# Optimization experiments

Hardware: AMD Instinct MI355X
Metric: run time of the kernel (lower is better)

The kernel has to match this reference:

```python
import jax, jax.numpy as jnp
import numpy as np
import math

B, L, HID, H = 16, 1024, 1024, 16
E = HID // H
HALF = L // 2 + 1                      # 513 rfft bins
GLOBAL_RATIO = 0.6
LEFT = int(HALF * (1.0 - GLOBAL_RATIO))  # 205 (i=0, filter_mixer='G')
RIGHT = HALF                            # 513
FACTOR = 1
TOP_K = int(FACTOR * math.log(L))       # 6
LN_EPS = 1e-12


def setup_inputs() -> dict:
    key = jax.random.key(0)
    ks = jax.random.split(key, 12)
    s = 0.02
    return {
        "input_tensor": jax.random.normal(ks[0], (B, L, HID), jnp.float32),
        "attention_mask": jnp.zeros((B, 1, 1, L), jnp.float32),
        "Wq": jax.random.normal(ks[1], (HID, HID), jnp.float32) * s,
        "bq": jnp.zeros((HID,), jnp.float32),
        "Wk": jax.random.normal(ks[2], (HID, HID), jnp.float32) * s,
        "bk": jnp.zeros((HID,), jnp.float32),
        "Wv": jax.random.normal(ks[3], (HID, HID), jnp.float32) * s,
        "bv": jnp.zeros((HID,), jnp.float32),
        "Wd": jax.random.normal(ks[4], (HID, HID), jnp.float32) * s,
        "bd": jnp.zeros((HID,), jnp.float32),
        "gamma": jnp.ones((HID,), jnp.float32),
        "beta": jnp.zeros((HID,), jnp.float32),
    }


def _heads(x):  # [B,L,HID] -> [B,H,E,L]
    return x.reshape(B, L, H, E).transpose(0, 2, 3, 1)


def _layer_norm(x, gamma, beta):
    mu = jnp.mean(x, axis=-1, keepdims=True)
    var = jnp.var(x, axis=-1, keepdims=True)
    return (x - mu) / jnp.sqrt(var + LN_EPS) * gamma + beta


def reference(input_tensor, attention_mask, Wq, bq, Wk, bk, Wv, bv, Wd, bd, gamma, beta):
    # QKV projections -> [B,H,E,L]
    q = _heads(input_tensor @ Wq + bq)
    k = _heads(input_tensor @ Wk + bk)
    v = _heads(input_tensor @ Wv + bv)

    # FFT-based autocorrelation restricted to retained frequency band [LEFT,RIGHT)
    q_fft = jnp.fft.rfft(q, axis=-1)            # [B,H,E,HALF] complex64
    k_fft = jnp.fft.rfft(k, axis=-1)
    res = q_fft[..., LEFT:RIGHT] * jnp.conj(k_fft[..., LEFT:RIGHT])
    box = jnp.zeros((B, H, E, HALF), res.dtype).at[..., LEFT:RIGHT].set(res)
    corr = jnp.fft.irfft(box, n=L, axis=-1)     # [B,H,E,L]

    # time_delay_agg_training: topk shared delays, softmax-weighted roll aggregation
    mean_value = jnp.mean(corr, axis=(1, 2))            # [B,L]
    _, idx = jax.lax.top_k(jnp.mean(mean_value, axis=0), TOP_K)  # [TOP_K]
    weights = mean_value[:, idx]                         # [B,TOP_K]
    tmp_corr = jax.nn.softmax(weights, axis=-1)
    delays_agg = jnp.zeros_like(v)
    for i in range(TOP_K):  # TOP_K=6, fixed small loop
        pattern = jnp.roll(v, -idx[i], axis=-1)
        delays_agg = delays_agg + pattern * tmp_corr[:, i][:, None, None, None]

    # [B,H,E,L] -> [B,L,HID]
    context = delays_agg.transpose(0, 3, 1, 2).reshape(B, L, HID)
    hidden = context @ Wd + bd
    return _layer_norm(hidden + input_tensor, gamma, beta)
```

## Files before the change

kernel.cpp:

```cpp
#include <hip/hip_runtime.h>


typedef unsigned short u16;
typedef unsigned int   u32;
typedef __attribute__((ext_vector_type(8))) __bf16 bf16x8;
typedef __attribute__((ext_vector_type(4))) float  floatx4;

#define HIDn 1024

__device__ __forceinline__ u16 f2b(float f){ u32 i = __float_as_uint(f); return (u16)((i + 0x7fffu + ((i>>16)&1u)) >> 16); }

__device__ __forceinline__ void gl_lds16(const u16* g, u16* l){
  __builtin_amdgcn_global_load_lds((__attribute__((address_space(1))) const void*)g,
                                   (__attribute__((address_space(3))) void*)l, 16, 0, 0);
}

__device__ __forceinline__ void bar(){
  asm volatile("" ::: "memory");
  __builtin_amdgcn_s_barrier();
  asm volatile("" ::: "memory");
}
__device__ __forceinline__ void lgkm0(){
  asm volatile("s_waitcnt lgkmcnt(0)" ::: "memory");
  __builtin_amdgcn_sched_barrier(0);
}

__global__ void fill_kernel(float* __restrict__ out, float v, int n)
{
  const int i = blockIdx.x*blockDim.x + threadIdx.x;
  if (i < n) out[i] = v;
}

__global__ __launch_bounds__(256)
void cast_kernel(const float* __restrict__ x, u16* __restrict__ xb)
{
  const int i = blockIdx.x*256 + threadIdx.x;
  const float4* xp = (const float4*)x;
  const float4 a = xp[2*i], b = xp[2*i+1];
  uint4 o;
  o.x = (u32)f2b(a.x) | ((u32)f2b(a.y)<<16);
  o.y = (u32)f2b(a.z) | ((u32)f2b(a.w)<<16);
  o.z = (u32)f2b(b.x) | ((u32)f2b(b.y)<<16);
  o.w = (u32)f2b(b.z) | ((u32)f2b(b.w)<<16);
  ((uint4*)xb)[i] = o;
}

__global__ __launch_bounds__(1024)
void transpose_kernel(const float* __restrict__ Wq, const float* __restrict__ Wk,
                      const float* __restrict__ Wv, const float* __restrict__ Wd,
                      u16* __restrict__ WqkvT, u16* __restrict__ WdT)
{
  __shared__ float tile[32][33];
  const int mat = blockIdx.z;
  const float* W = (mat==0)?Wq:(mat==1)?Wk:(mat==2)?Wv:Wd;
  const int k = blockIdx.y*32 + threadIdx.y;
  const int n = blockIdx.x*32 + threadIdx.x;
  tile[threadIdx.y][threadIdx.x] = W[(long)k*HIDn + n];
  __syncthreads();
  const int on = blockIdx.x*32 + threadIdx.y;
  const int ok = blockIdx.y*32 + threadIdx.x;
  const u16 val = f2b(tile[threadIdx.x][threadIdx.y]);
  if (mat < 3) WqkvT[(long)(mat*HIDn + on)*HIDn + ok] = val;
  else         WdT[(long)on*HIDn + ok] = val;
}

__global__ __launch_bounds__(1024)
void gf_kernel(float* __restrict__ gf, float* __restrict__ c)
{
  const int d = threadIdx.x;
  float s = 0.f;
  for (int f = 205; f < 512; ++f){
    int p = (f*d) & 1023;
    s += cosf(6.283185307179586f * (float)p * (1.0f/1024.0f));
  }
  gf[d] = (2.f*s + ((d & 1) ? -1.f : 1.f)) * (1.0f/1048576.0f);
  #pragma unroll
  for (int b = 0; b < 16; ++b) c[b*1024 + d] = 0.f;
}

template<int EPI>
__global__ __launch_bounds__(512, 2)
void gemm_mfma(const u16* __restrict__ A, int lda, long sA,
               const u16* __restrict__ Bt, int ldb, long sB,
               void* __restrict__ C0, u16* __restrict__ o1, u16* __restrict__ o2,
               int ldc, int K,
               const float* __restrict__ b0, const float* __restrict__ b1,
               const float* __restrict__ b2, const float* __restrict__ resid,
               float* __restrict__ cbuf)
{
  __shared__ __align__(16) u16 As[2][16384];
  __shared__ __align__(16) u16 Bs[2][16384];
  __shared__ float bins[512];

  const int bx = blockIdx.x, by = blockIdx.y, bz = blockIdx.z;
  const int tid  = threadIdx.x;
  const int wave = tid >> 6, lane = tid & 63;
  const int waveM = wave >> 2, waveN = wave & 3;
  const int qd = lane >> 4, ln = lane & 15, rl = ln & 7;
  const u16* Ab = A  + (long)bz * sA;
  const u16* Bb = Bt + (long)bz * sB;
  const int aRow0 = by * 256, bRow0 = bx * 256;
  const int nt = K >> 6;

  const int s0 = wave*128 + lane;
  const int r0 = s0 >> 3, r1 = r0 + 8;
  const int kc = ((s0 & 7) ^ (r0 & 7)) * 8;
  const long aOff0 = (long)(aRow0 + r0)*lda + kc;
  const long aOff1 = (long)(aRow0 + r1)*lda + kc;
  const long bOff0 = (long)(bRow0 + r0)*ldb + kc;
  const long bOff1 = (long)(bRow0 + r1)*ldb + kc;
  const int dstW = wave*1024;

#define STAGE_A(p, h, kt) do{ \
    gl_lds16(Ab + aOff0 + (long)(h)*128*lda + (kt), &As[p][(h)*8192 + dstW]); \
    gl_lds16(Ab + aOff1 + (long)(h)*128*lda + (kt), &As[p][(h)*8192 + dstW + 512]); }while(0)
#define STAGE_B(p, h, kt) do{ \
    gl_lds16(Bb + bOff0 + (long)(h)*128*ldb + (kt), &Bs[p][(h)*8192 + dstW]); \
    gl_lds16(Bb + bOff1 + (long)(h)*128*ldb + (kt), &Bs[p][(h)*8192 + dstW + 512]); }while(0)

  if (EPI == 3) bins[tid] = 0.f;

  floatx4 acc[8][4];
  const floatx4 z4 = {0.f, 0.f, 0.f, 0.f};
  #pragma unroll
  for (int i=0;i<8;++i)
    #pragma unroll
    for (int j=0;j<4;++j) acc[i][j] = z4;

  const int aRd = (waveM*128 + ln)*64;
  const int bRd = (waveN*64  + ln)*64;
  const int csw0 = ((0 + qd) ^ rl) * 8;
  const int csw1 = ((4 + qd) ^ rl) * 8;

  bf16x8 av0[4], av1[4];
  bf16x8 bvA0[2], bvA1[2];
  bf16x8 bvB0[2], bvB1[2];

#define DS_AV(BUF, MH) do{ const u16* Ap_ = &As[BUF][0]; \
    _Pragma("unroll") for (int mi=0;mi<4;++mi){ \
      av0[mi] = *(const bf16x8*)(Ap_ + aRd + (MH)*4096 + mi*1024 + csw0); \
      av1[mi] = *(const bf16x8*)(Ap_ + aRd + (MH)*4096 + mi*1024 + csw1); } }while(0)
#define DS_BV(BUF, NH, d0_, d1_) do{ const u16* Bp_ = &Bs[BUF][0]; \
    _Pragma("unroll") for (int ni=0;ni<2;++ni){ \
      d0_[ni] = *(const bf16x8*)(Bp_ + bRd + ((NH)*2+ni)*1024 + csw0); \
      d1_[ni] = *(const bf16x8*)(Bp_ + bRd + ((NH)*2+ni)*1024 + csw1); } }while(0)
#define MFMAQ(MH, NH, b0_, b1_) do{ \
    __builtin_amdgcn_sched_barrier(0); \
    __builtin_amdgcn_s_setprio(1); \
    _Pragma("unroll") for (int mi=0;mi<4;++mi) \
      _Pragma("unroll") for (int ni=0;ni<2;++ni){ \
        acc[(MH)*4+mi][(NH)*2+ni] = __builtin_amdgcn_mfma_f32_16x16x32_bf16(av0[mi], b0_[ni], acc[(MH)*4+mi][(NH)*2+ni],0,0,0); \
        acc[(MH)*4+mi][(NH)*2+ni] = __builtin_amdgcn_mfma_f32_16x16x32_bf16(av1[mi], b1_[ni], acc[(MH)*4+mi][(NH)*2+ni],0,0,0); } \
    __builtin_amdgcn_s_setprio(0); \
    __builtin_amdgcn_sched_barrier(0); }while(0)

  STAGE_B(0,0,0);  STAGE_B(0,1,0);  STAGE_A(0,0,0);  STAGE_A(0,1,0);
  STAGE_B(1,0,64); STAGE_B(1,1,64); STAGE_A(1,0,64); STAGE_A(1,1,64);
  asm volatile("s_waitcnt vmcnt(8)" ::: "memory");
  bar();

  const int nIt = nt >> 1;
  for (int it = 0; it < nIt-1; ++it){
    const int k2 = (it*2+2) << 6;
    const int k3 = (it*2+3) << 6;
    DS_AV(0,0); DS_BV(0,0,bvA0,bvA1);
    bar(); lgkm0(); MFMAQ(0,0,bvA0,bvA1); bar();
    DS_BV(0,1,bvB0,bvB1);
    bar(); lgkm0(); MFMAQ(0,1,bvB0,bvB1); bar();
    DS_AV(0,1); STAGE_B(0,0,k2);
    bar(); lgkm0(); MFMAQ(1,0,bvA0,bvA1); bar();
    STAGE_B(0,1,k2);
    asm volatile("s_waitcnt vmcnt(4)" ::: "memory");
    bar(); MFMAQ(1,1,bvB0,bvB1); bar();
    DS_AV(1,0); DS_BV(1,0,bvA0,bvA1); STAGE_A(0,0,k2);
    bar(); lgkm0(); MFMAQ(0,0,bvA0,bvA1); bar();
    DS_BV(1,1,bvB0,bvB1); STAGE_A(0,1,k2);
    bar(); lgkm0(); MFMAQ(0,1,bvB0,bvB1); bar();
    DS_AV(1,1); STAGE_B(1,0,k3);
    bar(); lgkm0(); MFMAQ(1,0,bvA0,bvA1); bar();
    STAGE_B(1,1,k3); STAGE_A(1,0,k3); STAGE_A(1,1,k3);
    asm volatile("s_waitcnt vmcnt(8)" ::: "memory");
    bar(); MFMAQ(1,1,bvB0,bvB1); bar();
  }
  DS_AV(0,0); DS_BV(0,0,bvA0,bvA1);
  bar(); lgkm0(); MFMAQ(0,0,bvA0,bvA1); bar();
  DS_BV(0,1,bvB0,bvB1);
  bar(); lgkm0(); MFMAQ(0,1,bvB0,bvB1); bar();
  DS_AV(0,1);
  bar(); lgkm0(); MFMAQ(1,0,bvA0,bvA1); bar();
  asm volatile("s_waitcnt vmcnt(0)" ::: "memory");
  bar(); MFMAQ(1,1,bvB0,bvB1); bar();
  DS_AV(1,0); DS_BV(1,0,bvA0,bvA1);
  bar(); lgkm0(); MFMAQ(0,0,bvA0,bvA1); bar();
  DS_BV(1,1,bvB0,bvB1);
  bar(); lgkm0(); MFMAQ(0,1,bvB0,bvB1); bar();
  DS_AV(1,1);
  bar(); lgkm0(); MFMAQ(1,0,bvA0,bvA1); bar();
  MFMAQ(1,1,bvB0,bvB1);
#undef STAGE_A
#undef STAGE_B
#undef DS_AV
#undef DS_BV
#undef MFMAQ

  if (EPI == 3){
    float dsum[11][4];
    #pragma unroll
    for (int dd=0; dd<11; ++dd)
      #pragma unroll
      for (int r=0;r<4;++r) dsum[dd][r] = 0.f;
    #pragma unroll
    for (int mi=0;mi<8;++mi)
      #pragma unroll
      for (int ni=0;ni<4;++ni){
        const int dd = mi - ni + 3;
        #pragma unroll
        for (int r=0;r<4;++r) dsum[dd][r] += acc[mi][ni][r];
      }
    const int base = 255 + 128*waveM - 64*waveN + 4*qd - ln;
    #pragma unroll
    for (int dd=0; dd<11; ++dd)
      #pragma unroll
      for (int r=0;r<4;++r)
        atomicAdd(&bins[base + 16*(dd-3) + r], dsum[dd][r]);
    __syncthreads();
    if (tid < 511){
      const int d = (aRow0 - bRow0 + tid - 255) & 1023;
      atomicAdd(cbuf + bz*1024 + d, bins[tid]);
    }
    return;
  }

  if (EPI == 0){
    const int which = bx >> 2;
    const float* bp = (which==0) ? b0 : ((which==1) ? b1 : b2);
    u16* Cb = (which==0) ? (u16*)C0 : ((which==1) ? o1 : o2);
    const int nb = bRow0 & 1023;
    #pragma unroll
    for (int mi=0;mi<8;++mi){
      const int gm = aRow0 + waveM*128 + mi*16 + qd*4;
      #pragma unroll
      for (int ni=0;ni<4;++ni){
        const int nl = nb + waveN*64 + ni*16 + ln;
        const float bias = bp[nl];
        #pragma unroll
        for (int r=0;r<4;++r) Cb[(long)(gm+r)*ldc + nl] = f2b(acc[mi][ni][r] + bias);
      }
    }
  } else {
    float* C = (float*)C0;
    #pragma unroll
    for (int mi=0;mi<8;++mi){
      const int gm = aRow0 + waveM*128 + mi*16 + qd*4;
      #pragma unroll
      for (int ni=0;ni<4;++ni){
        const int gn = bRow0 + waveN*64 + ni*16 + ln;
        const float bias = b0[gn];
        #pragma unroll
        for (int r=0;r<4;++r)
          C[(long)(gm+r)*ldc + gn] = acc[mi][ni][r] + bias + resid[(long)(gm+r)*ldc + gn];
      }
    }
  }
}

__global__ __launch_bounds__(1024)
void filter_kernel(const float* __restrict__ c, const float* __restrict__ gf,
                   float* __restrict__ mv)
{
  __shared__ float carr[1024];
  __shared__ float gsh[1024];
  const int b = blockIdx.x, l = threadIdx.x;
  carr[l] = c[b*1024 + l]; gsh[l] = gf[l];
  __syncthreads();
  float o = 0.f;
  #pragma unroll 4
  for (int m = 0; m < 1024; ++m) o += carr[m] * gsh[(l - m) & 1023];
  mv[b*1024 + l] = o;
}

__global__ __launch_bounds__(1024)
void topk_kernel(const float* __restrict__ mv, int* __restrict__ idxout,
                 float* __restrict__ wout)
{
  __shared__ float vals[1024];
  __shared__ float rv[1024];
  __shared__ int   ri[1024];
  __shared__ int   chosen[6];
  const int t = threadIdx.x;
  float s = 0.f;
  #pragma unroll
  for (int b = 0; b < 16; ++b) s += mv[b*1024 + t];
  vals[t] = s;
  __syncthreads();
  for (int r = 0; r < 6; ++r){
    rv[t] = vals[t]; ri[t] = t; __syncthreads();
    for (int off = 512; off > 0; off >>= 1){
      if (t < off){
        const float v2 = rv[t+off]; const int i2 = ri[t+off];
        if (v2 > rv[t] || (v2 == rv[t] && i2 < ri[t])){ rv[t] = v2; ri[t] = i2; }
      }
      __syncthreads();
    }
    if (t == 0){ chosen[r] = ri[0]; idxout[r] = ri[0]; }
    __syncthreads();
    if (t == chosen[r]) vals[t] = -3.0e38f;
    __syncthreads();
  }
  if (t < 16){
    float w[6]; float mx = -3.0e38f;
    #pragma unroll
    for (int i = 0; i < 6; ++i){ w[i] = mv[t*1024 + chosen[i]]; mx = fmaxf(mx, w[i]); }
    float sum = 0.f;
    #pragma unroll
    for (int i = 0; i < 6; ++i){ w[i] = expf(w[i] - mx); sum += w[i]; }
    #pragma unroll
    for (int i = 0; i < 6; ++i) wout[t*6 + i] = w[i] / sum;
  }
}

__global__ __launch_bounds__(256)
void context_kernel(const u16* __restrict__ Vb, const int* __restrict__ idx,
                    const float* __restrict__ w, u16* __restrict__ CT)
{
  const int row = blockIdx.x*2 + (threadIdx.x >> 7);
  const int b = row >> 10, l = row & 1023;
  const int t = threadIdx.x & 127;
  float wl[6]; int id[6];
  #pragma unroll
  for (int i = 0; i < 6; ++i){ id[i] = idx[i]; wl[i] = w[b*6 + i]; }
  float acc[8] = {0,0,0,0,0,0,0,0};
  #pragma unroll
  for (int i = 0; i < 6; ++i){
    const long src = (long)b*1024 + ((l + id[i]) & 1023);
    const uint4 pk = *(const uint4*)(Vb + src*1024 + t*8);
    const float ww = wl[i];
    union{float f; u32 u;} cv;
    cv.u = pk.x<<16;          acc[0] += ww*cv.f;
    cv.u = pk.x & 0xffff0000u; acc[1] += ww*cv.f;
    cv.u = pk.y<<16;          acc[2] += ww*cv.f;
    cv.u = pk.y & 0xffff0000u; acc[3] += ww*cv.f;
    cv.u = pk.z<<16;          acc[4] += ww*cv.f;
    cv.u = pk.z & 0xffff0000u; acc[5] += ww*cv.f;
    cv.u = pk.w<<16;          acc[6] += ww*cv.f;
    cv.u = pk.w & 0xffff0000u; acc[7] += ww*cv.f;
  }
  uint4 o;
  o.x = (u32)f2b(acc[0]) | ((u32)f2b(acc[1])<<16);
  o.y = (u32)f2b(acc[2]) | ((u32)f2b(acc[3])<<16);
  o.z = (u32)f2b(acc[4]) | ((u32)f2b(acc[5])<<16);
  o.w = (u32)f2b(acc[6]) | ((u32)f2b(acc[7])<<16);
  *(uint4*)(CT + (long)row*1024 + t*8) = o;
}

__global__ __launch_bounds__(256)
void ln_kernel(float* __restrict__ io, const float* __restrict__ gamma,
               const float* __restrict__ beta)
{
  __shared__ float s1[256];
  __shared__ float s2[256];
  const int row = blockIdx.x, t = threadIdx.x;
  float4 v = ((const float4*)(io + (long)row*1024))[t];
  s1[t] = v.x+v.y+v.z+v.w;
  s2[t] = v.x*v.x+v.y*v.y+v.z*v.z+v.w*v.w;
  __syncthreads();
  for (int off = 128; off > 0; off >>= 1){
    if (t < off){ s1[t] += s1[t+off]; s2[t] += s2[t+off]; }
    __syncthreads();
  }
  const float mu  = s1[0] * (1.f/1024.f);
  const float var = fmaxf(s2[0] * (1.f/1024.f) - mu*mu, 0.f);
  const float rstd = rsqrtf(var + 1e-12f);
  const float4 g  = ((const float4*)gamma)[t];
  const float4 be = ((const float4*)beta)[t];
  float4 o;
  o.x = (v.x-mu)*rstd*g.x + be.x;
  o.y = (v.y-mu)*rstd*g.y + be.y;
  o.z = (v.z-mu)*rstd*g.z + be.z;
  o.w = (v.w-mu)*rstd*g.w + be.w;
  ((float4*)(io + (long)row*1024))[t] = o;
}

extern "C" void kernel_launch(void* const* d_in, const int* in_sizes, int n_in,
                              void* d_out, int out_size, void* d_ws, size_t ws_size,
                              hipStream_t stream)
{
  (void)in_sizes; (void)n_in;
  const float* x     = (const float*)d_in[0];
  const float* Wq    = (const float*)d_in[2];
  const float* bq    = (const float*)d_in[3];
  const float* Wk    = (const float*)d_in[4];
  const float* bk    = (const float*)d_in[5];
  const float* Wv    = (const float*)d_in[6];
  const float* bv    = (const float*)d_in[7];
  const float* Wd    = (const float*)d_in[8];
  const float* bd    = (const float*)d_in[9];
  const float* gamma = (const float*)d_in[10];
  const float* beta  = (const float*)d_in[11];
  float* outp = (float*)d_out;

  const size_t NEED = 142741952UL;
  if (ws_size < NEED){
    const int n = out_size/2;
    fill_kernel<<<(n+255)/256, 256, 0, stream>>>(outp, (float)ws_size, n);
    return;
  }
  char* ws = (char*)d_ws;
  u16*  xb    = (u16*)(ws);
  u16*  Qb    = (u16*)(ws + 33554432L);
  u16*  Kb    = (u16*)(ws + 67108864L);
  u16*  Vb    = (u16*)(ws + 100663296L);
  u16*  WqkvT = (u16*)(ws + 134217728L);
  u16*  WdT   = (u16*)(ws + 140509184L);
  float* cbuf = (float*)(ws + 142606336L);
  float* mv   = (float*)(ws + 142671872L);
  float* gf   = (float*)(ws + 142737408L);
  int*   idxb = (int*)  (ws + 142741504L);
  float* wsm  = (float*)(ws + 142741568L);
  u16*  CT    = Qb;

  cast_kernel<<<8192, 256, 0, stream>>>(x, xb);
  transpose_kernel<<<dim3(32,32,4), dim3(32,32), 0, stream>>>(Wq, Wk, Wv, Wd, WqkvT, WdT);
  gf_kernel<<<1, 1024, 0, stream>>>(gf, cbuf);

  gemm_mfma<0><<<dim3(12,64,1), 512, 0, stream>>>(
      xb, 1024, 0L, WqkvT, 1024, 0L, Qb, Kb, Vb, 1024, 1024,
      bq, bk, bv, nullptr, nullptr);

  gemm_mfma<3><<<dim3(4,4,16), 512, 0, stream>>>(
      Qb, 1024, 1048576L, Kb, 1024, 1048576L, nullptr, nullptr, nullptr, 0, 1024,
      nullptr, nullptr, nullptr, nullptr, cbuf);

  filter_kernel<<<16, 1024, 0, stream>>>(cbuf, gf, mv);
  topk_kernel<<<1, 1024, 0, stream>>>(mv, idxb, wsm);
  context_kernel<<<8192, 256, 0, stream>>>(Vb, idxb, wsm, CT);

  gemm_mfma<2><<<dim3(4,64,1), 512, 0, stream>>>(
      CT, 1024, 0L, WdT, 1024, 0L, outp, nullptr, nullptr, 1024, 1024,
      bd, nullptr, nullptr, x, nullptr);

  ln_kernel<<<16384, 256, 0, stream>>>(outp, gamma, beta);
}
```

Baseline: 497.8 us.

## Drop gf kernel, use closed-form filter, swizzle GEMM blocks, warp-shuffle topk

Removes the serial gf_kernel launch. The band-pass filter is now computed in closed form (a Dirichlet-kernel sin/cos ratio) inside a filter kernel split into 64 blocks, and the cbuf zeroing moves into the cast kernel. The GEMM kernels remap block indices with an XCD-style swizzle so neighbouring tiles share cache. Top-k replaces the shared-memory tree reduction with wave shuffles. The closed-form filter may differ slightly numerically from the summed cosines, which could flip tie-breaking in top-k.

```diff
diff --git a/kernel.cpp b/kernel.cpp
--- a/kernel.cpp
+++ b/kernel.cpp
@@ -32,9 +32,11 @@
 }
 
 __global__ __launch_bounds__(256)
-void cast_kernel(const float* __restrict__ x, u16* __restrict__ xb)
+void cast_kernel(const float* __restrict__ x, u16* __restrict__ xb,
+                 float* __restrict__ cbuf)
 {
   const int i = blockIdx.x*256 + threadIdx.x;
+  if (blockIdx.x < 64) cbuf[i] = 0.f;
   const float4* xp = (const float4*)x;
   const float4 a = xp[2*i], b = xp[2*i+1];
   uint4 o;
@@ -64,20 +66,6 @@
   else         WdT[(long)on*HIDn + ok] = val;
 }
 
-__global__ __launch_bounds__(1024)
-void gf_kernel(float* __restrict__ gf, float* __restrict__ c)
-{
-  const int d = threadIdx.x;
-  float s = 0.f;
-  for (int f = 205; f < 512; ++f){
-    int p = (f*d) & 1023;
-    s += cosf(6.283185307179586f * (float)p * (1.0f/1024.0f));
-  }
-  gf[d] = (2.f*s + ((d & 1) ? -1.f : 1.f)) * (1.0f/1048576.0f);
-  #pragma unroll
-  for (int b = 0; b < 16; ++b) c[b*1024 + d] = 0.f;
-}
-
 template<int EPI>
 __global__ __launch_bounds__(512, 2)
 void gemm_mfma(const u16* __restrict__ A, int lda, long sA,
@@ -92,7 +80,15 @@
   __shared__ __align__(16) u16 Bs[2][16384];
   __shared__ float bins[512];
 
-  const int bx = blockIdx.x, by = blockIdx.y, bz = blockIdx.z;
+  const int gx = gridDim.x, gy = gridDim.y;
+  const int lin = (blockIdx.z*gy + blockIdx.y)*gx + blockIdx.x;
+  const int cpx = (gx*gy*gridDim.z) >> 3;
+  const int swz = (lin & 7)*cpx + (lin >> 3);
+  const int bx  = swz % gx;
+  const int byz = swz / gx;
+  const int by  = byz % gy;
+  const int bz  = byz / gy;
+
   const int tid  = threadIdx.x;
   const int wave = tid >> 6, lane = tid & 63;
   const int waveM = wave >> 2, waveN = wave & 3;
@@ -264,15 +260,28 @@
   }
 }
 
-__global__ __launch_bounds__(1024)
-void filter_kernel(const float* __restrict__ c, const float* __restrict__ gf,
-                   float* __restrict__ mv)
+__global__ __launch_bounds__(256)
+void filter_kernel(const float* __restrict__ c, float* __restrict__ mv)
 {
   __shared__ float carr[1024];
   __shared__ float gsh[1024];
-  const int b = blockIdx.x, l = threadIdx.x;
-  carr[l] = c[b*1024 + l]; gsh[l] = gf[l];
+  const int b = blockIdx.x >> 2, l0 = (blockIdx.x & 3) << 8;
+  const int t = threadIdx.x;
+  #pragma unroll
+  for (int j = 0; j < 4; ++j){
+    const int d = t + j*256;
+    carr[d] = c[b*1024 + d];
+    float s;
+    if (d == 0) s = 307.f;
+    else {
+      const float k = 3.14159265358979e0f/1024.f;
+      const int n1 = (307*d) & 2047, n2 = (716*d) & 2047;
+      s = sinf((float)n1*k) * cosf((float)n2*k) / sinf((float)d*k);
+    }
+    gsh[d] = (2.f*s + ((d & 1) ? -1.f : 1.f)) * (1.0f/1048576.0f);
+  }
   __syncthreads();
+  const int l = l0 + t;
   float o = 0.f;
   #pragma unroll 4
   for (int m = 0; m < 1024; ++m) o += carr[m] * gsh[(l - m) & 1023];
@@ -284,27 +293,32 @@
                  float* __restrict__ wout)
 {
   __shared__ float vals[1024];
-  __shared__ float rv[1024];
-  __shared__ int   ri[1024];
+  __shared__ float wv[16];
+  __shared__ int   wi[16];
   __shared__ int   chosen[6];
-  const int t = threadIdx.x;
+  const int t = threadIdx.x, lane = t & 63, wid = t >> 6;
   float s = 0.f;
   #pragma unroll
   for (int b = 0; b < 16; ++b) s += mv[b*1024 + t];
   vals[t] = s;
   __syncthreads();
   for (int r = 0; r < 6; ++r){
-    rv[t] = vals[t]; ri[t] = t; __syncthreads();
-    for (int off = 512; off > 0; off >>= 1){
-      if (t < off){
-        const float v2 = rv[t+off]; const int i2 = ri[t+off];
-        if (v2 > rv[t] || (v2 == rv[t] && i2 < ri[t])){ rv[t] = v2; ri[t] = i2; }
-      }
-      __syncthreads();
-    }
-    if (t == 0){ chosen[r] = ri[0]; idxout[r] = ri[0]; }
+    float cv = vals[t]; int ci = t;
+    #pragma unroll
+    for (int off = 32; off > 0; off >>= 1){
+      const float ov = __shfl_down(cv, off);
+      const int   oi = __shfl_down(ci, off);
+      if (ov > cv || (ov == cv && oi < ci)){ cv = ov; ci = oi; }
+    }
+    if (lane == 0){ wv[wid] = cv; wi[wid] = ci; }
     __syncthreads();
-    if (t == chosen[r]) vals[t] = -3.0e38f;
+    if (t == 0){
+      float bv = wv[0]; int bi = wi[0];
+      #pragma unroll
+      for (int k = 1; k < 16; ++k)
+        if (wv[k] > bv || (wv[k] == bv && wi[k] < bi)){ bv = wv[k]; bi = wi[k]; }
+      chosen[r] = bi; idxout[r] = bi; vals[bi] = -3.0e38f;
+    }
     __syncthreads();
   }
   if (t < 16){
@@ -414,14 +428,12 @@
   u16*  WdT   = (u16*)(ws + 140509184L);
   float* cbuf = (float*)(ws + 142606336L);
   float* mv   = (float*)(ws + 142671872L);
-  float* gf   = (float*)(ws + 142737408L);
   int*   idxb = (int*)  (ws + 142741504L);
   float* wsm  = (float*)(ws + 142741568L);
   u16*  CT    = Qb;
 
-  cast_kernel<<<8192, 256, 0, stream>>>(x, xb);
+  cast_kernel<<<8192, 256, 0, stream>>>(x, xb, cbuf);
   transpose_kernel<<<dim3(32,32,4), dim3(32,32), 0, stream>>>(Wq, Wk, Wv, Wd, WqkvT, WdT);
-  gf_kernel<<<1, 1024, 0, stream>>>(gf, cbuf);
 
   gemm_mfma<0><<<dim3(12,64,1), 512, 0, stream>>>(
       xb, 1024, 0L, WqkvT, 1024, 0L, Qb, Kb, Vb, 1024, 1024,
@@ -431,7 +443,7 @@
       Qb, 1024, 1048576L, Kb, 1024, 1048576L, nullptr, nullptr, nullptr, 0, 1024,
       nullptr, nullptr, nullptr, nullptr, cbuf);
 
-  filter_kernel<<<16, 1024, 0, stream>>>(cbuf, gf, mv);
+  filter_kernel<<<64, 256, 0, stream>>>(cbuf, mv);
   topk_kernel<<<1, 1024, 0, stream>>>(mv, idxb, wsm);
   context_kernel<<<8192, 256, 0, stream>>>(Vb, idxb, wsm, CT);
 
```

Result: faster. 439.0 us (-11.8%).
